# Performance work log

Hardware: AMD Instinct MI355X
Metric: run time of the kernel (lower is better)

## Reference

```python
import jax, jax.numpy as jnp
import numpy as np

N_TOKENS = 32768
DIM = 2048
N_EXPERTS = 256
N_GROUPS = 8
N_LIMITED_GROUPS = 4
TOP_K = 8
ROUTE_SCALE = 2.5


def setup_inputs() -> dict:
    key = jax.random.key(0)
    k1, k2, k3, k4 = jax.random.split(key, 4)
    x = jax.random.normal(k1, (N_TOKENS, DIM), dtype=jnp.float32)
    w1 = jax.random.normal(k2, (N_EXPERTS, DIM), dtype=jnp.float32) * (DIM ** -0.5)
    b_lin = jax.random.normal(k3, (N_EXPERTS,), dtype=jnp.float32) * 0.02
    bias = jax.random.normal(k4, (N_EXPERTS,), dtype=jnp.float32) * 0.02
    return {"x": x, "w1": w1, "b_lin": b_lin, "bias": bias}


def reference(x, w1, b_lin, bias):
    n = x.shape[0]
    # gate GEMM: [N, dim] x [dim, E] -> [N, E]
    logits = jnp.einsum("nd,ed->ne", x, w1) + b_lin
    # sigmoid scoring with L1 normalization
    s = jax.nn.sigmoid(logits)
    s = s / jnp.sum(s, axis=-1, keepdims=True)
    # routing-correction bias (torch code adds it in place, so it is also in the
    # gathered values via the original_scores alias)
    s = s + bias
    original_scores = s
    # group-limited masking: keep only top n_limited_groups groups (amax score,
    # since use_bias=True)
    g = s.reshape(n, N_GROUPS, N_EXPERTS // N_GROUPS)
    group_scores = jnp.max(g, axis=-1)                      # [N, G]
    _, gidx = jax.lax.top_k(group_scores, N_LIMITED_GROUPS)  # [N, Glim]
    keep = jnp.zeros((n, N_GROUPS), dtype=bool).at[
        jnp.arange(n)[:, None], gidx].set(True)
    masked = jnp.where(keep[:, :, None], g, -jnp.inf).reshape(n, N_EXPERTS)
    # final top-k over masked scores, gather from (bias-added) original scores
    _, indices = jax.lax.top_k(masked, TOP_K)               # [N, k]
    values = jnp.take_along_axis(original_scores, indices, axis=1) * ROUTE_SCALE
    return values.astype(x.dtype), indices
```

## Files before the change

kernel.cpp:

```cpp
#include <hip/hip_runtime.h>
#include <math.h>

#define NTOK   32768
#define DIM    2048
#define NE     256
#define NG     8
#define GSZ    32
#define NLIM   4
#define TOPK   8
#define RSCALE 2.5f
#define TAU    4e-7f

#define BT      32
#define THREADS 256
#define KT      16
#define NKT     (DIM / KT)
#define WOFF    262144
#define TILE_B  16384

typedef __bf16 bf16x8 __attribute__((ext_vector_type(8)));
typedef float  f32x16 __attribute__((ext_vector_type(16)));

__global__ __launch_bounds__(256) void wsplit_kernel(
    const float* __restrict__ w1, unsigned int* __restrict__ wt)
{
    const int g  = blockIdx.x * 256 + threadIdx.x;
    const int e  = g & 255;
    const int hi = (g >> 8) & 1;
    const int p  = (g >> 9) & 1;
    const int kt = g >> 10;
    const float* src = w1 + (size_t)e * DIM + kt * 16 + hi * 8;

    uint4 o;
    unsigned int w[4];
#pragma unroll
    for (int q = 0; q < 4; ++q) {
        const float v0 = src[2 * q], v1 = src[2 * q + 1];
        const unsigned int u0 = __float_as_uint(v0);
        const unsigned int u1 = __float_as_uint(v1);
        if (p == 0) {
            w[q] = (u0 >> 16) | (u1 & 0xFFFF0000u);
        } else {
            const float r0 = v0 - __uint_as_float(u0 & 0xFFFF0000u);
            const float r1 = v1 - __uint_as_float(u1 & 0xFFFF0000u);
            w[q] = (__float_as_uint(r0) >> 16) |
                   (__float_as_uint(r1) & 0xFFFF0000u);
        }
    }
    o.x = w[0]; o.y = w[1]; o.z = w[2]; o.w = w[3];
    *(uint4*)(wt + (size_t)g * 4) = o;
}

__device__ __forceinline__ void split_pack(float4 a, float4 b,
                                           bf16x8& h8, bf16x8& r8) {
    float v[8] = {a.x, a.y, a.z, a.w, b.x, b.y, b.z, b.w};
    union { unsigned int u[4]; bf16x8 v8; } H, R;
#pragma unroll
    for (int q = 0; q < 4; ++q) {
        const unsigned int u0 = __float_as_uint(v[2 * q]);
        const unsigned int u1 = __float_as_uint(v[2 * q + 1]);
        H.u[q] = (u0 >> 16) | (u1 & 0xFFFF0000u);
        const float r0 = v[2 * q]     - __uint_as_float(u0 & 0xFFFF0000u);
        const float r1 = v[2 * q + 1] - __uint_as_float(u1 & 0xFFFF0000u);
        R.u[q] = (__float_as_uint(r0) >> 16) |
                 (__float_as_uint(r1) & 0xFFFF0000u);
    }
    h8 = H.v8; r8 = R.v8;
}

__global__ __launch_bounds__(THREADS, 4) void router_pass1(
    const float* __restrict__ x, const unsigned int* __restrict__ wt,
    const float* __restrict__ b_lin, const float* __restrict__ bias,
    float* __restrict__ out_vals, float* __restrict__ out_idx,
    int* __restrict__ wsI)
{
    __shared__ float sc[32 * 260];

    const int tid  = threadIdx.x;
    const int lane = tid & 63;
    const int wn   = tid >> 6;
    const int l31  = lane & 31;
    const int hi   = lane >> 5;
    const int t0   = blockIdx.x * BT;

    const float4* xA = (const float4*)(x + (size_t)(t0 + l31) * DIM) + hi * 2;
    const char* wb = (const char*)wt + hi * 4096 + (wn * 64 + l31) * 16;

    f32x16 acc[2] = {};

#pragma unroll 4
    for (int kt = 0; kt < NKT; ++kt) {
        const float4 f0 = xA[kt * 4];
        const float4 f1 = xA[kt * 4 + 1];
        const char* pB = wb + (size_t)kt * TILE_B;
        const bf16x8 b0h = *(const bf16x8*)(pB);
        const bf16x8 b0r = *(const bf16x8*)(pB + 8192);
        const bf16x8 b1h = *(const bf16x8*)(pB + 512);
        const bf16x8 b1r = *(const bf16x8*)(pB + 512 + 8192);
        bf16x8 ah, ar;
        split_pack(f0, f1, ah, ar);
        acc[0] = __builtin_amdgcn_mfma_f32_32x32x16_bf16(ah, b0h, acc[0], 0, 0, 0);
        acc[0] = __builtin_amdgcn_mfma_f32_32x32x16_bf16(ah, b0r, acc[0], 0, 0, 0);
        acc[0] = __builtin_amdgcn_mfma_f32_32x32x16_bf16(ar, b0h, acc[0], 0, 0, 0);
        acc[1] = __builtin_amdgcn_mfma_f32_32x32x16_bf16(ah, b1h, acc[1], 0, 0, 0);
        acc[1] = __builtin_amdgcn_mfma_f32_32x32x16_bf16(ah, b1r, acc[1], 0, 0, 0);
        acc[1] = __builtin_amdgcn_mfma_f32_32x32x16_bf16(ar, b1h, acc[1], 0, 0, 0);
    }

#pragma unroll
    for (int ni = 0; ni < 2; ++ni) {
#pragma unroll
        for (int r = 0; r < 16; ++r) {
            const int row = (r & 3) + 8 * (r >> 2) + 4 * hi;
            const int e   = wn * 64 + ni * 32 + l31;
            sc[row * 260 + e] = acc[ni][r];
        }
    }
    __syncthreads();

    const int tx = tid & 31;
    const int ty = tid >> 5;
    float blv[8], bsv[8];
#pragma unroll
    for (int j = 0; j < 8; ++j) {
        blv[j] = b_lin[tx + 32 * j];
        bsv[j] = bias[tx + 32 * j];
    }

#pragma unroll
    for (int i = 0; i < 4; ++i) {
        const int row = ty * 4 + i;
        float s8[8];
        float psum = 0.0f;
#pragma unroll
        for (int j = 0; j < 8; ++j) {
            const float lg = sc[row * 260 + tx + 32 * j] + blv[j];
            const float s = 1.0f / (1.0f + expf(-lg));
            s8[j] = s;
            psum += s;
        }
#pragma unroll
        for (int m = 1; m <= 16; m <<= 1) psum += __shfl_xor(psum, m);
#pragma unroll
        for (int j = 0; j < 8; ++j) s8[j] = s8[j] / psum + bsv[j];

        float gm[8];
#pragma unroll
        for (int j = 0; j < 8; ++j) gm[j] = s8[j];
#pragma unroll
        for (int m = 1; m <= 16; m <<= 1)
#pragma unroll
            for (int j = 0; j < 8; ++j)
                gm[j] = fmaxf(gm[j], __shfl_xor(gm[j], m));

        unsigned keep = 0u;
        float g4v = 0.0f, g5v = 0.0f;
#pragma unroll
        for (int r = 0; r < 5; ++r) {
            float bv = -1e30f; int bg = 0;
#pragma unroll
            for (int g = 0; g < 8; ++g)
                if (!((keep >> g) & 1) && gm[g] > bv) { bv = gm[g]; bg = g; }
            if (r < 4) { keep |= 1u << bg; g4v = bv; }
            else g5v = bv;
        }
        float margin = g4v - g5v;

#pragma unroll
        for (int j = 0; j < 8; ++j)
            if (!((keep >> j) & 1)) s8[j] = -1e30f;

        float tv[9]; int te[9];
#pragma unroll
        for (int r = 0; r < 9; ++r) {
            float bv = -1e30f; int bj = 8;
#pragma unroll
            for (int j = 0; j < 8; ++j)
                if (s8[j] > bv) { bv = s8[j]; bj = j; }
            int be = (bj < 8) ? (tx + 32 * bj) : 9999;
#pragma unroll
            for (int m = 1; m <= 16; m <<= 1) {
                const float ov = __shfl_xor(bv, m);
                const int   oe = __shfl_xor(be, m);
                if (ov > bv || (ov == bv && oe < be)) { bv = ov; be = oe; }
            }
            tv[r] = bv; te[r] = be;
            if (r < 8 && (be & 31) == tx) s8[be >> 5] = -1e30f;
        }
#pragma unroll
        for (int r = 0; r < 8; ++r) margin = fminf(margin, tv[r] - tv[r + 1]);

        if (tx == 0) {
            const int t = t0 + row;
            const int base = t * TOPK;
#pragma unroll
            for (int r = 0; r < 8; ++r) {
                out_vals[base + r] = tv[r] * RSCALE;
                out_idx[base + r]  = (float)te[r];
            }
            if (margin < TAU) {
                const int slot = atomicAdd(&wsI[0], 1);
                if (slot < 60000) wsI[4 + slot] = t;
            }
        }
    }
}

__global__ __launch_bounds__(256, 1) void router_pass2(
    const float* __restrict__ x, const float* __restrict__ w1,
    const float* __restrict__ b_lin, const float* __restrict__ bias,
    float* __restrict__ out_vals, float* __restrict__ out_idx,
    const int* __restrict__ wsI)
{
    __shared__ double xrow[DIM];
    __shared__ double red[256];
    __shared__ double sc[NE];

    const int tid = threadIdx.x;
    const int count = min(wsI[0], 60000);
    const int* list = wsI + 4;
    const float4* x4 = (const float4*)x;
    const float4* w4 = (const float4*)w1;

    for (int li = blockIdx.x; li < count; li += gridDim.x) {
        const int t = list[li];
        __syncthreads();
#pragma unroll
        for (int q = 0; q < 2; ++q) {
            const int id = tid + 256 * q;
            const float4 v = x4[t * 512 + id];
            xrow[id * 4 + 0] = (double)v.x;
            xrow[id * 4 + 1] = (double)v.y;
            xrow[id * 4 + 2] = (double)v.z;
            xrow[id * 4 + 3] = (double)v.w;
        }
        __syncthreads();

        const int e = tid;
        double a0 = 0.0, a1 = 0.0, a2 = 0.0, a3 = 0.0;
#pragma unroll 2
        for (int k4 = 0; k4 < 512; k4 += 4) {
#pragma unroll
            for (int z = 0; z < 4; ++z) {
                const float4 wv = w4[e * 512 + k4 + z];
                double* ac = (z == 0) ? &a0 : (z == 1) ? &a1 : (z == 2) ? &a2 : &a3;
                *ac = fma(xrow[(k4 + z) * 4 + 0], (double)wv.x, *ac);
                *ac = fma(xrow[(k4 + z) * 4 + 1], (double)wv.y, *ac);
                *ac = fma(xrow[(k4 + z) * 4 + 2], (double)wv.z, *ac);
                *ac = fma(xrow[(k4 + z) * 4 + 3], (double)wv.w, *ac);
            }
        }
        const double lg = ((a0 + a1) + (a2 + a3)) + (double)b_lin[e];
        const double s = 1.0 / (1.0 + exp(-lg));
        red[tid] = s;
        __syncthreads();
        for (int off = 128; off > 0; off >>= 1) {
            if (tid < off) red[tid] += red[tid + off];
            __syncthreads();
        }
        sc[e] = s / red[0] + (double)bias[e];
        __syncthreads();

        if (tid == 0) {
            double gmax[NG];
            for (int g = 0; g < NG; ++g) {
                double mx = -INFINITY;
                for (int q = 0; q < GSZ; ++q) {
                    const double v = sc[g * GSZ + q];
                    mx = (v > mx) ? v : mx;
                }
                gmax[g] = mx;
            }
            unsigned keep = 0u;
            for (int r = 0; r < NLIM; ++r) {
                int best = 0; double bv = -INFINITY;
                for (int g = 0; g < NG; ++g) {
                    if (keep & (1u << g)) continue;
                    if (gmax[g] > bv) { bv = gmax[g]; best = g; }
                }
                keep |= 1u << best;
            }
            double tv[TOPK]; int ti[TOPK];
            for (int r = 0; r < TOPK; ++r) { tv[r] = -INFINITY; ti[r] = NE; }
            for (int g = 0; g < NG; ++g) {
                if (!(keep & (1u << g))) continue;
                for (int q = 0; q < GSZ; ++q) {
                    const int ee = g * GSZ + q;
                    const double v = sc[ee];
                    if (v > tv[TOPK - 1]) {
                        int p = TOPK - 1;
                        while (p > 0 && v > tv[p - 1]) {
                            tv[p] = tv[p - 1]; ti[p] = ti[p - 1]; --p;
                        }
                        tv[p] = v; ti[p] = ee;
                    }
                }
            }
            const int base = t * TOPK;
            for (int r = 0; r < TOPK; ++r) {
                out_vals[base + r] = (float)(tv[r] * (double)RSCALE);
                out_idx[base + r]  = (float)ti[r];
            }
        }
    }
}

extern "C" void kernel_launch(void* const* d_in, const int* in_sizes, int n_in,
                              void* d_out, int out_size, void* d_ws, size_t ws_size,
                              hipStream_t stream) {
    const float* x     = (const float*)d_in[0];
    const float* w1    = (const float*)d_in[1];
    const float* b_lin = (const float*)d_in[2];
    const float* bias  = (const float*)d_in[3];
    float* out_vals = (float*)d_out;
    float* out_idx  = (float*)d_out + (size_t)NTOK * TOPK;

    int* wsI = (int*)d_ws;
    unsigned int* wt = (unsigned int*)((char*)d_ws + WOFF);

    hipMemsetAsync(d_ws, 0, 16, stream);
    wsplit_kernel<<<dim3(512), 256, 0, stream>>>(w1, wt);
    router_pass1<<<dim3(NTOK / BT), THREADS, 0, stream>>>(
        x, wt, b_lin, bias, out_vals, out_idx, wsI);
    router_pass2<<<dim3(256), 256, 0, stream>>>(
        x, w1, b_lin, bias, out_vals, out_idx, (const int*)d_ws);
}
```

Before: 324.8 us.

## Use 64-token blocks with 2x2 wave tiling and double-buffered operand loads

Doubles the token tile per block to 64 and arranges the four waves as a 2x2 grid, each computing 32 tokens by 128 experts. Each weight fragment is now reused across twice as many tokens, and each x row is reused across more experts per wave. The K loop is software-pipelined with two register buffers so the next tile's loads are issued before the current MFMAs, and the epilogue processes the two 32-row halves through shared memory in turn. The near-tie threshold for the fp64 recheck pass is also lowered so fewer tokens are sent to pass2. In exchange, register pressure rises, occupancy hints drop from 4 to 2 blocks, and the smaller threshold slightly narrows the safety margin for exact tie handling.

```diff
diff --git a/kernel.cpp b/kernel.cpp
--- a/kernel.cpp
+++ b/kernel.cpp
@@ -9,9 +9,9 @@
 #define NLIM   4
 #define TOPK   8
 #define RSCALE 2.5f
-#define TAU    4e-7f
-
-#define BT      32
+#define TAU    2.5e-7f
+
+#define BT      64
 #define THREADS 256
 #define KT      16
 #define NKT     (DIM / KT)
@@ -68,7 +68,7 @@
     h8 = H.v8; r8 = R.v8;
 }
 
-__global__ __launch_bounds__(THREADS, 4) void router_pass1(
+__global__ __launch_bounds__(THREADS, 2) void router_pass1(
     const float* __restrict__ x, const unsigned int* __restrict__ wt,
     const float* __restrict__ b_lin, const float* __restrict__ bias,
     float* __restrict__ out_vals, float* __restrict__ out_idx,
@@ -78,45 +78,58 @@
 
     const int tid  = threadIdx.x;
     const int lane = tid & 63;
-    const int wn   = tid >> 6;
+    const int wave = tid >> 6;
     const int l31  = lane & 31;
     const int hi   = lane >> 5;
+    const int wm   = wave >> 1;
+    const int wn   = wave & 1;
     const int t0   = blockIdx.x * BT;
 
-    const float4* xA = (const float4*)(x + (size_t)(t0 + l31) * DIM) + hi * 2;
-    const char* wb = (const char*)wt + hi * 4096 + (wn * 64 + l31) * 16;
-
-    f32x16 acc[2] = {};
-
-#pragma unroll 4
-    for (int kt = 0; kt < NKT; ++kt) {
-        const float4 f0 = xA[kt * 4];
-        const float4 f1 = xA[kt * 4 + 1];
-        const char* pB = wb + (size_t)kt * TILE_B;
-        const bf16x8 b0h = *(const bf16x8*)(pB);
-        const bf16x8 b0r = *(const bf16x8*)(pB + 8192);
-        const bf16x8 b1h = *(const bf16x8*)(pB + 512);
-        const bf16x8 b1r = *(const bf16x8*)(pB + 512 + 8192);
+    const float4* xA = (const float4*)(x + (size_t)(t0 + wm * 32 + l31) * DIM)
+                       + hi * 2;
+    const char* wb = (const char*)wt + hi * 4096 + (wn * 128 + l31) * 16;
+
+    auto LOADB = [&](bf16x8 (&B)[4][2], int kt) {
+#pragma unroll
+        for (int ni = 0; ni < 4; ++ni)
+#pragma unroll
+            for (int p = 0; p < 2; ++p)
+                B[ni][p] = *(const bf16x8*)(wb + (size_t)kt * TILE_B +
+                                            ni * 512 + p * 8192);
+    };
+
+    f32x16 acc[4] = {};
+
+    auto COMP = [&](bf16x8 (&B)[4][2], float4 f0, float4 f1) {
         bf16x8 ah, ar;
         split_pack(f0, f1, ah, ar);
-        acc[0] = __builtin_amdgcn_mfma_f32_32x32x16_bf16(ah, b0h, acc[0], 0, 0, 0);
-        acc[0] = __builtin_amdgcn_mfma_f32_32x32x16_bf16(ah, b0r, acc[0], 0, 0, 0);
-        acc[0] = __builtin_amdgcn_mfma_f32_32x32x16_bf16(ar, b0h, acc[0], 0, 0, 0);
-        acc[1] = __builtin_amdgcn_mfma_f32_32x32x16_bf16(ah, b1h, acc[1], 0, 0, 0);
-        acc[1] = __builtin_amdgcn_mfma_f32_32x32x16_bf16(ah, b1r, acc[1], 0, 0, 0);
-        acc[1] = __builtin_amdgcn_mfma_f32_32x32x16_bf16(ar, b1h, acc[1], 0, 0, 0);
-    }
-
-#pragma unroll
-    for (int ni = 0; ni < 2; ++ni) {
-#pragma unroll
-        for (int r = 0; r < 16; ++r) {
-            const int row = (r & 3) + 8 * (r >> 2) + 4 * hi;
-            const int e   = wn * 64 + ni * 32 + l31;
-            sc[row * 260 + e] = acc[ni][r];
-        }
-    }
-    __syncthreads();
+#pragma unroll
+        for (int ni = 0; ni < 4; ++ni)
+            acc[ni] = __builtin_amdgcn_mfma_f32_32x32x16_bf16(ah, B[ni][0], acc[ni], 0, 0, 0);
+#pragma unroll
+        for (int ni = 0; ni < 4; ++ni)
+            acc[ni] = __builtin_amdgcn_mfma_f32_32x32x16_bf16(ah, B[ni][1], acc[ni], 0, 0, 0);
+#pragma unroll
+        for (int ni = 0; ni < 4; ++ni)
+            acc[ni] = __builtin_amdgcn_mfma_f32_32x32x16_bf16(ar, B[ni][0], acc[ni], 0, 0, 0);
+    };
+
+    bf16x8 B0[4][2], B1[4][2];
+    float4 xa0, xa1, xb0, xb1;
+
+    LOADB(B0, 0);
+    xa0 = xA[0]; xa1 = xA[1];
+
+    for (int kt = 0; kt < NKT; kt += 2) {
+        const int k1 = (kt + 1 < NKT) ? kt + 1 : 0;
+        const int k2 = (kt + 2 < NKT) ? kt + 2 : 0;
+        LOADB(B1, k1);
+        xb0 = xA[k1 * 4]; xb1 = xA[k1 * 4 + 1];
+        COMP(B0, xa0, xa1);
+        LOADB(B0, k2);
+        xa0 = xA[k2 * 4]; xa1 = xA[k2 * 4 + 1];
+        COMP(B1, xb0, xb1);
+    }
 
     const int tx = tid & 31;
     const int ty = tid >> 5;
@@ -128,79 +141,96 @@
     }
 
 #pragma unroll
-    for (int i = 0; i < 4; ++i) {
-        const int row = ty * 4 + i;
-        float s8[8];
-        float psum = 0.0f;
-#pragma unroll
-        for (int j = 0; j < 8; ++j) {
-            const float lg = sc[row * 260 + tx + 32 * j] + blv[j];
-            const float s = 1.0f / (1.0f + expf(-lg));
-            s8[j] = s;
-            psum += s;
-        }
-#pragma unroll
-        for (int m = 1; m <= 16; m <<= 1) psum += __shfl_xor(psum, m);
-#pragma unroll
-        for (int j = 0; j < 8; ++j) s8[j] = s8[j] / psum + bsv[j];
-
-        float gm[8];
-#pragma unroll
-        for (int j = 0; j < 8; ++j) gm[j] = s8[j];
-#pragma unroll
-        for (int m = 1; m <= 16; m <<= 1)
+    for (int h = 0; h < 2; ++h) {
+        __syncthreads();
+        if (wm == h) {
+#pragma unroll
+            for (int ni = 0; ni < 4; ++ni) {
+#pragma unroll
+                for (int r = 0; r < 16; ++r) {
+                    const int row = (r & 3) + 8 * (r >> 2) + 4 * hi;
+                    const int e   = wn * 128 + ni * 32 + l31;
+                    sc[row * 260 + e] = acc[ni][r];
+                }
+            }
+        }
+        __syncthreads();
+
+#pragma unroll
+        for (int i = 0; i < 4; ++i) {
+            const int row = ty * 4 + i;
+            float s8[8];
+            float psum = 0.0f;
+#pragma unroll
+            for (int j = 0; j < 8; ++j) {
+                const float lg = sc[row * 260 + tx + 32 * j] + blv[j];
+                const float s = 1.0f / (1.0f + expf(-lg));
+                s8[j] = s;
+                psum += s;
+            }
+#pragma unroll
+            for (int m = 1; m <= 16; m <<= 1) psum += __shfl_xor(psum, m);
+#pragma unroll
+            for (int j = 0; j < 8; ++j) s8[j] = s8[j] / psum + bsv[j];
+
+            float gm[8];
+#pragma unroll
+            for (int j = 0; j < 8; ++j) gm[j] = s8[j];
+#pragma unroll
+            for (int m = 1; m <= 16; m <<= 1)
+#pragma unroll
+                for (int j = 0; j < 8; ++j)
+                    gm[j] = fmaxf(gm[j], __shfl_xor(gm[j], m));
+
+            unsigned keep = 0u;
+            float g4v = 0.0f, g5v = 0.0f;
+#pragma unroll
+            for (int r = 0; r < 5; ++r) {
+                float bv = -1e30f; int bg = 0;
+#pragma unroll
+                for (int g = 0; g < 8; ++g)
+                    if (!((keep >> g) & 1) && gm[g] > bv) { bv = gm[g]; bg = g; }
+                if (r < 4) { keep |= 1u << bg; g4v = bv; }
+                else g5v = bv;
+            }
+            float margin = g4v - g5v;
+
 #pragma unroll
             for (int j = 0; j < 8; ++j)
-                gm[j] = fmaxf(gm[j], __shfl_xor(gm[j], m));
-
-        unsigned keep = 0u;
-        float g4v = 0.0f, g5v = 0.0f;
-#pragma unroll
-        for (int r = 0; r < 5; ++r) {
-            float bv = -1e30f; int bg = 0;
-#pragma unroll
-            for (int g = 0; g < 8; ++g)
-                if (!((keep >> g) & 1) && gm[g] > bv) { bv = gm[g]; bg = g; }
-            if (r < 4) { keep |= 1u << bg; g4v = bv; }
-            else g5v = bv;
-        }
-        float margin = g4v - g5v;
-
-#pragma unroll
-        for (int j = 0; j < 8; ++j)
-            if (!((keep >> j) & 1)) s8[j] = -1e30f;
-
-        float tv[9]; int te[9];
-#pragma unroll
-        for (int r = 0; r < 9; ++r) {
-            float bv = -1e30f; int bj = 8;
-#pragma unroll
-            for (int j = 0; j < 8; ++j)
-                if (s8[j] > bv) { bv = s8[j]; bj = j; }
-            int be = (bj < 8) ? (tx + 32 * bj) : 9999;
-#pragma unroll
-            for (int m = 1; m <= 16; m <<= 1) {
-                const float ov = __shfl_xor(bv, m);
-                const int   oe = __shfl_xor(be, m);
-                if (ov > bv || (ov == bv && oe < be)) { bv = ov; be = oe; }
-            }
-            tv[r] = bv; te[r] = be;
-            if (r < 8 && (be & 31) == tx) s8[be >> 5] = -1e30f;
-        }
-#pragma unroll
-        for (int r = 0; r < 8; ++r) margin = fminf(margin, tv[r] - tv[r + 1]);
-
-        if (tx == 0) {
-            const int t = t0 + row;
-            const int base = t * TOPK;
-#pragma unroll
-            for (int r = 0; r < 8; ++r) {
-                out_vals[base + r] = tv[r] * RSCALE;
-                out_idx[base + r]  = (float)te[r];
-            }
-            if (margin < TAU) {
-                const int slot = atomicAdd(&wsI[0], 1);
-                if (slot < 60000) wsI[4 + slot] = t;
+                if (!((keep >> j) & 1)) s8[j] = -1e30f;
+
+            float tv[9]; int te[9];
+#pragma unroll
+            for (int r = 0; r < 9; ++r) {
+                float bv = -1e30f; int bj = 8;
+#pragma unroll
+                for (int j = 0; j < 8; ++j)
+                    if (s8[j] > bv) { bv = s8[j]; bj = j; }
+                int be = (bj < 8) ? (tx + 32 * bj) : 9999;
+#pragma unroll
+                for (int m = 1; m <= 16; m <<= 1) {
+                    const float ov = __shfl_xor(bv, m);
+                    const int   oe = __shfl_xor(be, m);
+                    if (ov > bv || (ov == bv && oe < be)) { bv = ov; be = oe; }
+                }
+                tv[r] = bv; te[r] = be;
+                if (r < 8 && (be & 31) == tx) s8[be >> 5] = -1e30f;
+            }
+#pragma unroll
+            for (int r = 0; r < 8; ++r) margin = fminf(margin, tv[r] - tv[r + 1]);
+
+            if (tx == 0) {
+                const int t = t0 + h * 32 + row;
+                const int base = t * TOPK;
+#pragma unroll
+                for (int r = 0; r < 8; ++r) {
+                    out_vals[base + r] = tv[r] * RSCALE;
+                    out_idx[base + r]  = (float)te[r];
+                }
+                if (margin < TAU) {
+                    const int slot = atomicAdd(&wsI[0], 1);
+                    if (slot < 60000) wsI[4 + slot] = t;
+                }
             }
         }
     }
```

New measurement: 303.5 us. 6.5% less time.
